# Kernel optimization log

Measured on AMD Instinct MI355X. Metric: run time of the kernel, lower is better.

The kernel has to match this reference:

```python
import jax, jax.numpy as jnp
import numpy as np


def setup_inputs() -> dict:
    key = jax.random.key(0)
    ks = jax.random.split(key, 11)
    b, c, h, w = 16, 64, 16, 16
    F = 64  # num_filters
    O = 64  # num_outputs
    d_in = 2 * (c + 1)  # 130: concat of two (feature + coord) vectors
    s = 0.05
    return {
        "x_img": jax.random.normal(ks[0], (b, c, h, w), dtype=jnp.float32),
        "Wg0": jax.random.normal(ks[1], (F, d_in), dtype=jnp.float32) * s,
        "bg0": jax.random.normal(ks[2], (F,), dtype=jnp.float32) * s,
        "Wg1": jax.random.normal(ks[3], (F, F), dtype=jnp.float32) * s,
        "bg1": jax.random.normal(ks[4], (F,), dtype=jnp.float32) * s,
        "Wg2": jax.random.normal(ks[5], (F, F), dtype=jnp.float32) * s,
        "bg2": jax.random.normal(ks[6], (F,), dtype=jnp.float32) * s,
        "Wp": jax.random.normal(ks[7], (F, F), dtype=jnp.float32) * s,
        "bp": jax.random.normal(ks[8], (F,), dtype=jnp.float32) * s,
        "Wo": jax.random.normal(ks[9], (O, F), dtype=jnp.float32) * s,
        "bo": jax.random.normal(ks[10], (O,), dtype=jnp.float32) * s,
    }


def reference(x_img, Wg0, bg0, Wg1, bg1, Wg2, bg2, Wp, bp, Wo, bo):
    b, c, h, w = x_img.shape
    L = h * w
    # [b, L, c]: flatten spatial, move channels last
    feats = x_img.reshape(b, c, L).transpose(0, 2, 1)
    # append 1-d coordinate feature -> [b, L, c+1]
    coord = jnp.broadcast_to(
        jnp.arange(L, dtype=feats.dtype).reshape(1, L, 1), (b, L, 1)
    )
    feats = jnp.concatenate([feats, coord], axis=2)
    # pairwise broadcast-concat: pair[b, p, q] = [feats[b, q], feats[b, p]]
    d = feats.shape[-1]
    x_i = jnp.broadcast_to(feats[:, None, :, :], (b, L, L, d))
    x_j = jnp.broadcast_to(feats[:, :, None, :], (b, L, L, d))
    pair = jnp.concatenate([x_i, x_j], axis=3)  # [b, L, L, 2*(c+1)]
    # shared g-MLP (3 layers, ReLU)
    out = jax.nn.relu(jnp.einsum("bpqd,fd->bpqf", pair, Wg0) + bg0)
    out = jax.nn.relu(jnp.einsum("bpqf,gf->bpqg", out, Wg1) + bg1)
    out = jax.nn.relu(jnp.einsum("bpqf,gf->bpqg", out, Wg2) + bg2)
    # sum-reduce over both pair dims -> [b, F]
    out = out.sum(axis=(1, 2))
    # f-network
    out = jax.nn.relu(out @ Wp.T + bp)
    out = out @ Wo.T + bo
    return out
```

## Files before the change

kernel.cpp:

```cpp
#include <hip/hip_runtime.h>


typedef short s8v __attribute__((ext_vector_type(8)));
typedef float f4v __attribute__((ext_vector_type(4)));

#define LDA 68
#define LDY 72

__device__ __forceinline__ short bfr(float v) {
  return __builtin_bit_cast(short, (__bf16)v);
}

__global__ __launch_bounds__(256) void k_pre(
    const float* __restrict__ x, const float* __restrict__ Wg0,
    const float* __restrict__ bg0, float* __restrict__ Ag,
    float* __restrict__ Bg, float* __restrict__ Sg) {
  __shared__ float ws[64 * 131];
  __shared__ float xs[64 * 17];

  const int t = threadIdx.x;
  const int b = blockIdx.x >> 4;
  const int l0 = (blockIdx.x & 15) * 16;

  if (blockIdx.x == 0) {
    for (int i = t; i < 16 * 64; i += 256) Sg[i] = 0.f;
  }
  for (int i = t; i < 64 * 130; i += 256) {
    int f = i / 130, d = i - f * 130;
    ws[f * 131 + d] = Wg0[i];
  }
  for (int i = t; i < 64 * 16; i += 256) {
    int ch = i >> 4, li = i & 15;
    xs[ch * 17 + li] = x[b * 16384 + ch * 256 + l0 + li];
  }
  __syncthreads();

  const int f = t & 63;
  const int w = t >> 6;
  float accA[4] = {0.f, 0.f, 0.f, 0.f};
  float accB[4] = {0.f, 0.f, 0.f, 0.f};
  for (int d = 0; d < 64; ++d) {
    float wa = ws[f * 131 + d];
    float wb = ws[f * 131 + 65 + d];
#pragma unroll
    for (int i = 0; i < 4; ++i) {
      float xv = xs[d * 17 + w + 4 * i];
      accA[i] += xv * wa;
      accB[i] += xv * wb;
    }
  }
  const float wca = ws[f * 131 + 64];
  const float wcb = ws[f * 131 + 129];
  const float bias = bg0[f];
#pragma unroll
  for (int i = 0; i < 4; ++i) {
    int l = l0 + w + 4 * i;
    Ag[(b * 256 + l) * 64 + f] = accA[i] + (float)l * wca;
    Bg[(b * 256 + l) * 64 + f] = accB[i] + (float)l * wcb + bias;
  }
}

__global__ __launch_bounds__(256, 2) void k_main(
    const float* __restrict__ Ag, const float* __restrict__ Bg,
    const float* __restrict__ Wg1, const float* __restrict__ bg1,
    const float* __restrict__ Wg2, const float* __restrict__ bg2,
    float* __restrict__ Sg) {
  __shared__ __align__(16) float As[256 * LDA];
  __shared__ __align__(16) short Y1s[4][16 * LDY];
  __shared__ float Sblk[64];

  const int t = threadIdx.x;
  const int wid = t >> 6;
  const int lane = t & 63;
  const int mm = lane & 15;
  const int quad = lane >> 4;
  const int b = blockIdx.y;
  const int p0 = blockIdx.x * 8;

  if (t < 64) Sblk[t] = 0.f;

  const float4* Ab4 = (const float4*)(Ag + b * 16384);
  for (int i = 0; i < 16; ++i) {
    int flat4 = t + 256 * i;
    int q = flat4 >> 4, c4 = flat4 & 15;
    float4 v = Ab4[flat4];
    *(float4*)&As[q * LDA + c4 * 4] = v;
  }

  s8v W1f[4][2], W2f[4][2];
  float bg1v[4], bg2v[4];
#pragma unroll
  for (int gt = 0; gt < 4; ++gt) {
    bg1v[gt] = bg1[gt * 16 + mm];
    bg2v[gt] = bg2[gt * 16 + mm];
#pragma unroll
    for (int kh = 0; kh < 2; ++kh) {
      const float* r1 = Wg1 + (gt * 16 + mm) * 64 + kh * 32 + quad * 8;
      const float* r2 = Wg2 + (gt * 16 + mm) * 64 + kh * 32 + quad * 8;
      s8v w1, w2;
#pragma unroll
      for (int j = 0; j < 8; ++j) { w1[j] = bfr(r1[j]); w2[j] = bfr(r2[j]); }
      W1f[gt][kh] = w1;
      W2f[gt][kh] = w2;
    }
  }
  __syncthreads();

  float cs[4] = {0.f, 0.f, 0.f, 0.f};
  short* Y1w = Y1s[wid];
  const float* Bb = Bg + (b * 256 + p0) * 64;

  const float4* Bp4 = (const float4*)Bb;
  float4 bq0 = Bp4[quad * 2],     bq1 = Bp4[quad * 2 + 1];
  float4 bq2 = Bp4[8 + quad * 2], bq3 = Bp4[9 + quad * 2];

  for (int ip = 0; ip < 8; ++ip) {
    const int pn = (ip < 7) ? ip + 1 : 7;
    const float4* Bn4 = (const float4*)(Bb + pn * 64);
    float4 bn0 = Bn4[quad * 2],     bn1 = Bn4[quad * 2 + 1];
    float4 bn2 = Bn4[8 + quad * 2], bn3 = Bn4[9 + quad * 2];

#pragma unroll
    for (int qt = 0; qt < 4; ++qt) {
      const float* arow = &As[(wid * 64 + qt * 16 + mm) * LDA];
      float4 a0 = *(const float4*)(arow + quad * 8);
      float4 a1 = *(const float4*)(arow + quad * 8 + 4);
      float4 a2 = *(const float4*)(arow + 32 + quad * 8);
      float4 a3 = *(const float4*)(arow + 36 + quad * 8);
      s8v x0, x1;
      x0[0] = bfr(fmaxf(a0.x + bq0.x, 0.f));
      x0[1] = bfr(fmaxf(a0.y + bq0.y, 0.f));
      x0[2] = bfr(fmaxf(a0.z + bq0.z, 0.f));
      x0[3] = bfr(fmaxf(a0.w + bq0.w, 0.f));
      x0[4] = bfr(fmaxf(a1.x + bq1.x, 0.f));
      x0[5] = bfr(fmaxf(a1.y + bq1.y, 0.f));
      x0[6] = bfr(fmaxf(a1.z + bq1.z, 0.f));
      x0[7] = bfr(fmaxf(a1.w + bq1.w, 0.f));
      x1[0] = bfr(fmaxf(a2.x + bq2.x, 0.f));
      x1[1] = bfr(fmaxf(a2.y + bq2.y, 0.f));
      x1[2] = bfr(fmaxf(a2.z + bq2.z, 0.f));
      x1[3] = bfr(fmaxf(a2.w + bq2.w, 0.f));
      x1[4] = bfr(fmaxf(a3.x + bq3.x, 0.f));
      x1[5] = bfr(fmaxf(a3.y + bq3.y, 0.f));
      x1[6] = bfr(fmaxf(a3.z + bq3.z, 0.f));
      x1[7] = bfr(fmaxf(a3.w + bq3.w, 0.f));

      f4v acc1[4];
#pragma unroll
      for (int gt = 0; gt < 4; ++gt) {
        f4v c = {bg1v[gt], bg1v[gt], bg1v[gt], bg1v[gt]};
        c = __builtin_amdgcn_mfma_f32_16x16x32_bf16(x0, W1f[gt][0], c, 0, 0, 0);
        c = __builtin_amdgcn_mfma_f32_16x16x32_bf16(x1, W1f[gt][1], c, 0, 0, 0);
        acc1[gt] = c;
      }
#pragma unroll
      for (int gt = 0; gt < 4; ++gt) {
#pragma unroll
        for (int r = 0; r < 4; ++r)
          Y1w[(quad * 4 + r) * LDY + gt * 16 + mm] = bfr(fmaxf(acc1[gt][r], 0.f));
      }
      s8v y0 = *(const s8v*)(Y1w + mm * LDY + quad * 8);
      s8v y1 = *(const s8v*)(Y1w + mm * LDY + 32 + quad * 8);
#pragma unroll
      for (int gt = 0; gt < 4; ++gt) {
        f4v c = {bg2v[gt], bg2v[gt], bg2v[gt], bg2v[gt]};
        c = __builtin_amdgcn_mfma_f32_16x16x32_bf16(y0, W2f[gt][0], c, 0, 0, 0);
        c = __builtin_amdgcn_mfma_f32_16x16x32_bf16(y1, W2f[gt][1], c, 0, 0, 0);
        cs[gt] += fmaxf(c[0], 0.f) + fmaxf(c[1], 0.f) +
                  fmaxf(c[2], 0.f) + fmaxf(c[3], 0.f);
      }
    }
    bq0 = bn0; bq1 = bn1; bq2 = bn2; bq3 = bn3;
  }

#pragma unroll
  for (int gt = 0; gt < 4; ++gt) {
    float v = cs[gt];
    v += __shfl_xor(v, 16);
    v += __shfl_xor(v, 32);
    if (lane < 16) atomicAdd(&Sblk[gt * 16 + lane], v);
  }
  __syncthreads();
  if (t < 64) atomicAdd(&Sg[b * 64 + t], Sblk[t]);
}

__global__ __launch_bounds__(64) void k_final(
    const float* __restrict__ S, const float* __restrict__ Wp,
    const float* __restrict__ bp, const float* __restrict__ Wo,
    const float* __restrict__ bo, float* __restrict__ out) {
  __shared__ float sv[64], tv[64];
  const int b = blockIdx.x, t = threadIdx.x;
  sv[t] = S[b * 64 + t];
  __syncthreads();
  float acc = bp[t];
  for (int g = 0; g < 64; ++g) acc += sv[g] * Wp[t * 64 + g];
  tv[t] = fmaxf(acc, 0.f);
  __syncthreads();
  float o = bo[t];
  for (int f = 0; f < 64; ++f) o += tv[f] * Wo[t * 64 + f];
  out[b * 64 + t] = o;
}

extern "C" void kernel_launch(void* const* d_in, const int* in_sizes, int n_in,
                              void* d_out, int out_size, void* d_ws, size_t ws_size,
                              hipStream_t stream) {
  const float* x   = (const float*)d_in[0];
  const float* Wg0 = (const float*)d_in[1];
  const float* bg0 = (const float*)d_in[2];
  const float* Wg1 = (const float*)d_in[3];
  const float* bg1 = (const float*)d_in[4];
  const float* Wg2 = (const float*)d_in[5];
  const float* bg2 = (const float*)d_in[6];
  const float* Wp  = (const float*)d_in[7];
  const float* bp  = (const float*)d_in[8];
  const float* Wo  = (const float*)d_in[9];
  const float* bo  = (const float*)d_in[10];
  float* out = (float*)d_out;

  float* Ag = (float*)d_ws;
  float* Bg = Ag + 16 * 256 * 64;
  float* Sg = Bg + 16 * 256 * 64;

  k_pre<<<256, 256, 0, stream>>>(x, Wg0, bg0, Ag, Bg, Sg);
  k_main<<<dim3(32, 16), 256, 0, stream>>>(Ag, Bg, Wg1, bg1, Wg2, bg2, Sg);
  k_final<<<16, 64, 0, stream>>>(Sg, Wp, bp, Wo, bo, out);
}
```

Before: 114.3 us.

## Keep A tile in registers, swap MFMA operands, regrid main kernel over p-blocks

The main kernel no longer stages the whole per-batch A matrix (256x64 floats) in LDS. Each wave instead holds one 16-row q-tile of A in registers and loops over 32 p rows, with the grid split into p-groups times q-groups. MFMA operands are swapped so weights are the A operand, which makes layer-1 outputs transposed. Those outputs can then be written to LDS as packed bf16 pairs and bias loads become vectorized. This removes the large LDS footprint and the per-block redundant A loads, trading them for more blocks that each reload weights and A rows and do a heavier final shuffle reduction.

```diff
diff --git a/kernel.cpp b/kernel.cpp
--- a/kernel.cpp
+++ b/kernel.cpp
@@ -4,11 +4,28 @@
 typedef short s8v __attribute__((ext_vector_type(8)));
 typedef float f4v __attribute__((ext_vector_type(4)));
 
-#define LDA 68
-#define LDY 72
+#define LDYB 72
 
 __device__ __forceinline__ short bfr(float v) {
   return __builtin_bit_cast(short, (__bf16)v);
+}
+__device__ __forceinline__ unsigned pkbf(float a, float b) {
+  unsigned lo = (unsigned short)__builtin_bit_cast(unsigned short, (__bf16)a);
+  unsigned hi = (unsigned short)__builtin_bit_cast(unsigned short, (__bf16)b);
+  return lo | (hi << 16);
+}
+__device__ __forceinline__ f4v relu4(f4v v) {
+  f4v z = {0.f, 0.f, 0.f, 0.f};
+  return __builtin_elementwise_max(v, z);
+}
+__device__ __forceinline__ s8v cvt8(f4v a, f4v b) {
+  s8v r;
+  r[0] = bfr(a[0]); r[1] = bfr(a[1]); r[2] = bfr(a[2]); r[3] = bfr(a[3]);
+  r[4] = bfr(b[0]); r[5] = bfr(b[1]); r[6] = bfr(b[2]); r[7] = bfr(b[3]);
+  return r;
+}
+__device__ __forceinline__ f4v ldf4(const float* p) {
+  return *(const f4v*)p;
 }
 
 __global__ __launch_bounds__(256) void k_pre(
@@ -65,8 +82,7 @@
     const float* __restrict__ Wg1, const float* __restrict__ bg1,
     const float* __restrict__ Wg2, const float* __restrict__ bg2,
     float* __restrict__ Sg) {
-  __shared__ __align__(16) float As[256 * LDA];
-  __shared__ __align__(16) short Y1s[4][16 * LDY];
+  __shared__ __align__(16) short Ys[4][16 * LDYB];
   __shared__ float Sblk[64];
 
   const int t = threadIdx.x;
@@ -75,24 +91,24 @@
   const int mm = lane & 15;
   const int quad = lane >> 4;
   const int b = blockIdx.y;
-  const int p0 = blockIdx.x * 8;
+  const int qg = blockIdx.x & 3;
+  const int p0 = (blockIdx.x >> 2) * 32;
+  const int q0 = (qg * 4 + wid) * 16;
 
   if (t < 64) Sblk[t] = 0.f;
 
-  const float4* Ab4 = (const float4*)(Ag + b * 16384);
-  for (int i = 0; i < 16; ++i) {
-    int flat4 = t + 256 * i;
-    int q = flat4 >> 4, c4 = flat4 & 15;
-    float4 v = Ab4[flat4];
-    *(float4*)&As[q * LDA + c4 * 4] = v;
-  }
+  const float* Arow = Ag + (b * 256 + q0 + mm) * 64;
+  f4v af0 = ldf4(Arow + quad * 8);
+  f4v af1 = ldf4(Arow + quad * 8 + 4);
+  f4v af2 = ldf4(Arow + 32 + quad * 8);
+  f4v af3 = ldf4(Arow + 36 + quad * 8);
 
   s8v W1f[4][2], W2f[4][2];
-  float bg1v[4], bg2v[4];
+  f4v c1i[4], c2i[4];
 #pragma unroll
   for (int gt = 0; gt < 4; ++gt) {
-    bg1v[gt] = bg1[gt * 16 + mm];
-    bg2v[gt] = bg2[gt * 16 + mm];
+    c1i[gt] = ldf4(bg1 + gt * 16 + quad * 4);
+    c2i[gt] = ldf4(bg2 + gt * 16 + quad * 4);
 #pragma unroll
     for (int kh = 0; kh < 2; ++kh) {
       const float* r1 = Wg1 + (gt * 16 + mm) * 64 + kh * 32 + quad * 8;
@@ -106,79 +122,62 @@
   }
   __syncthreads();
 
-  float cs[4] = {0.f, 0.f, 0.f, 0.f};
-  short* Y1w = Y1s[wid];
+  short* Yw = Ys[wid];
   const float* Bb = Bg + (b * 256 + p0) * 64;
-
-  const float4* Bp4 = (const float4*)Bb;
-  float4 bq0 = Bp4[quad * 2],     bq1 = Bp4[quad * 2 + 1];
-  float4 bq2 = Bp4[8 + quad * 2], bq3 = Bp4[9 + quad * 2];
-
-  for (int ip = 0; ip < 8; ++ip) {
-    const int pn = (ip < 7) ? ip + 1 : 7;
-    const float4* Bn4 = (const float4*)(Bb + pn * 64);
-    float4 bn0 = Bn4[quad * 2],     bn1 = Bn4[quad * 2 + 1];
-    float4 bn2 = Bn4[8 + quad * 2], bn3 = Bn4[9 + quad * 2];
-
-#pragma unroll
-    for (int qt = 0; qt < 4; ++qt) {
-      const float* arow = &As[(wid * 64 + qt * 16 + mm) * LDA];
-      float4 a0 = *(const float4*)(arow + quad * 8);
-      float4 a1 = *(const float4*)(arow + quad * 8 + 4);
-      float4 a2 = *(const float4*)(arow + 32 + quad * 8);
-      float4 a3 = *(const float4*)(arow + 36 + quad * 8);
-      s8v x0, x1;
-      x0[0] = bfr(fmaxf(a0.x + bq0.x, 0.f));
-      x0[1] = bfr(fmaxf(a0.y + bq0.y, 0.f));
-      x0[2] = bfr(fmaxf(a0.z + bq0.z, 0.f));
-      x0[3] = bfr(fmaxf(a0.w + bq0.w, 0.f));
-      x0[4] = bfr(fmaxf(a1.x + bq1.x, 0.f));
-      x0[5] = bfr(fmaxf(a1.y + bq1.y, 0.f));
-      x0[6] = bfr(fmaxf(a1.z + bq1.z, 0.f));
-      x0[7] = bfr(fmaxf(a1.w + bq1.w, 0.f));
-      x1[0] = bfr(fmaxf(a2.x + bq2.x, 0.f));
-      x1[1] = bfr(fmaxf(a2.y + bq2.y, 0.f));
-      x1[2] = bfr(fmaxf(a2.z + bq2.z, 0.f));
-      x1[3] = bfr(fmaxf(a2.w + bq2.w, 0.f));
-      x1[4] = bfr(fmaxf(a3.x + bq3.x, 0.f));
-      x1[5] = bfr(fmaxf(a3.y + bq3.y, 0.f));
-      x1[6] = bfr(fmaxf(a3.z + bq3.z, 0.f));
-      x1[7] = bfr(fmaxf(a3.w + bq3.w, 0.f));
-
-      f4v acc1[4];
-#pragma unroll
-      for (int gt = 0; gt < 4; ++gt) {
-        f4v c = {bg1v[gt], bg1v[gt], bg1v[gt], bg1v[gt]};
-        c = __builtin_amdgcn_mfma_f32_16x16x32_bf16(x0, W1f[gt][0], c, 0, 0, 0);
-        c = __builtin_amdgcn_mfma_f32_16x16x32_bf16(x1, W1f[gt][1], c, 0, 0, 0);
-        acc1[gt] = c;
-      }
-#pragma unroll
-      for (int gt = 0; gt < 4; ++gt) {
-#pragma unroll
-        for (int r = 0; r < 4; ++r)
-          Y1w[(quad * 4 + r) * LDY + gt * 16 + mm] = bfr(fmaxf(acc1[gt][r], 0.f));
-      }
-      s8v y0 = *(const s8v*)(Y1w + mm * LDY + quad * 8);
-      s8v y1 = *(const s8v*)(Y1w + mm * LDY + 32 + quad * 8);
-#pragma unroll
-      for (int gt = 0; gt < 4; ++gt) {
-        f4v c = {bg2v[gt], bg2v[gt], bg2v[gt], bg2v[gt]};
-        c = __builtin_amdgcn_mfma_f32_16x16x32_bf16(y0, W2f[gt][0], c, 0, 0, 0);
-        c = __builtin_amdgcn_mfma_f32_16x16x32_bf16(y1, W2f[gt][1], c, 0, 0, 0);
-        cs[gt] += fmaxf(c[0], 0.f) + fmaxf(c[1], 0.f) +
-                  fmaxf(c[2], 0.f) + fmaxf(c[3], 0.f);
-      }
-    }
+  f4v cs[4] = {{0.f,0.f,0.f,0.f},{0.f,0.f,0.f,0.f},
+               {0.f,0.f,0.f,0.f},{0.f,0.f,0.f,0.f}};
+
+  f4v bq0 = ldf4(Bb + quad * 8);
+  f4v bq1 = ldf4(Bb + quad * 8 + 4);
+  f4v bq2 = ldf4(Bb + 32 + quad * 8);
+  f4v bq3 = ldf4(Bb + 36 + quad * 8);
+
+  for (int ip = 0; ip < 32; ++ip) {
+    const float* Bn = Bb + ((ip < 31) ? ip + 1 : 31) * 64;
+    f4v bn0 = ldf4(Bn + quad * 8);
+    f4v bn1 = ldf4(Bn + quad * 8 + 4);
+    f4v bn2 = ldf4(Bn + 32 + quad * 8);
+    f4v bn3 = ldf4(Bn + 36 + quad * 8);
+
+    s8v x0 = cvt8(relu4(af0 + bq0), relu4(af1 + bq1));
+    s8v x1 = cvt8(relu4(af2 + bq2), relu4(af3 + bq3));
+
+#pragma unroll
+    for (int gt = 0; gt < 4; ++gt) {
+      f4v a = c1i[gt];
+      a = __builtin_amdgcn_mfma_f32_16x16x32_bf16(W1f[gt][0], x0, a, 0, 0, 0);
+      a = __builtin_amdgcn_mfma_f32_16x16x32_bf16(W1f[gt][1], x1, a, 0, 0, 0);
+      a = relu4(a);
+      unsigned d0 = pkbf(a[0], a[1]);
+      unsigned d1 = pkbf(a[2], a[3]);
+      *(uint2*)&Yw[mm * LDYB + gt * 16 + quad * 4] = make_uint2(d0, d1);
+    }
+
+    s8v y0 = *(const s8v*)&Yw[mm * LDYB + quad * 8];
+    s8v y1 = *(const s8v*)&Yw[mm * LDYB + 32 + quad * 8];
+
+#pragma unroll
+    for (int ot = 0; ot < 4; ++ot) {
+      f4v a = c2i[ot];
+      a = __builtin_amdgcn_mfma_f32_16x16x32_bf16(W2f[ot][0], y0, a, 0, 0, 0);
+      a = __builtin_amdgcn_mfma_f32_16x16x32_bf16(W2f[ot][1], y1, a, 0, 0, 0);
+      cs[ot] += relu4(a);
+    }
+
     bq0 = bn0; bq1 = bn1; bq2 = bn2; bq3 = bn3;
   }
 
 #pragma unroll
-  for (int gt = 0; gt < 4; ++gt) {
-    float v = cs[gt];
-    v += __shfl_xor(v, 16);
-    v += __shfl_xor(v, 32);
-    if (lane < 16) atomicAdd(&Sblk[gt * 16 + lane], v);
+  for (int ot = 0; ot < 4; ++ot) {
+#pragma unroll
+    for (int r = 0; r < 4; ++r) {
+      float v = cs[ot][r];
+      v += __shfl_xor(v, 1);
+      v += __shfl_xor(v, 2);
+      v += __shfl_xor(v, 4);
+      v += __shfl_xor(v, 8);
+      if (mm == 0) atomicAdd(&Sblk[ot * 16 + quad * 4 + r], v);
+    }
   }
   __syncthreads();
   if (t < 64) atomicAdd(&Sg[b * 64 + t], Sblk[t]);
```

After: 119.1 us. +4.2%, slower.
